# Optimization experiments

Measured on AMD Instinct MI355X. Metric: run time of the kernel, lower is better.

Reference implementation:

```python
import jax, jax.numpy as jnp
import numpy as np

N_NODES = 100_000
N_EDGES = 1_600_000
IN_CH = 16
OUT_CH = 64


def _init_linear(key, fan_in, fan_out):
    kw, kb = jax.random.split(key)
    bound = 1.0 / np.sqrt(fan_in)
    w = jax.random.uniform(kw, (fan_in, fan_out), jnp.float32, -bound, bound)
    b = jax.random.uniform(kb, (fan_out,), jnp.float32, -bound, bound)
    return w, b


def setup_inputs() -> dict:
    key = jax.random.key(0)
    ks = jax.random.split(key, 8)
    x = jax.random.normal(ks[0], (N_NODES, IN_CH), jnp.float32)
    pos = jax.random.normal(ks[1], (N_NODES, 3), jnp.float32)
    edge_index = jax.random.randint(ks[2], (2, N_EDGES), 0, N_NODES, jnp.int64)
    # local_nn: [in+3, 64, 128, out], ReLU after each linear
    w1, b1 = _init_linear(ks[3], IN_CH + 3, 64)
    w2, b2 = _init_linear(ks[4], 64, 128)
    w3, b3 = _init_linear(ks[5], 128, OUT_CH)
    # global_nn: [out, out]
    wg, bg = _init_linear(ks[6], OUT_CH, OUT_CH)
    return {"x": x, "pos": pos, "w1": w1, "b1": b1, "w2": w2, "b2": b2,
            "w3": w3, "b3": b3, "wg": wg, "bg": bg, "edge_index": edge_index}


def reference(x, pos, w1, b1, w2, b2, w3, b3, wg, bg, edge_index):
    src = edge_index[0]  # j (source / neighbor)
    dst = edge_index[1]  # i (target / center)
    # per-edge message input: [x_j, pos_j - pos_i]  -> [E, in+3]
    rel_pos = pos[src] - pos[dst]
    msg = jnp.concatenate([x[src], rel_pos], axis=-1)
    # local MLP (Linear -> ReLU chain)
    h = jax.nn.relu(msg @ w1 + b1)
    h = jax.nn.relu(h @ w2 + b2)
    h = jax.nn.relu(h @ w3 + b3)  # [E, out]
    # max aggregation over incoming edges per target node
    agg = jax.ops.segment_max(h, dst, num_segments=N_NODES)
    agg = jnp.where(jnp.isfinite(agg), agg, 0.0)  # isolated nodes -> 0
    # global MLP
    out = jax.nn.relu(agg @ wg + bg)  # [N, out]
    return out
```

## Files before the change

### kernel.cpp

```cpp
#include <hip/hip_runtime.h>


typedef __attribute__((ext_vector_type(8))) _Float16 half8;
typedef __attribute__((ext_vector_type(4))) float floatx4;

#define RELU(v) fmaxf((v), 0.0f)
#define LDS_FENCE() asm volatile("s_waitcnt lgkmcnt(0)" ::: "memory")

__global__ void count_prep_kernel(const int* __restrict__ ei, int E,
                                  int* __restrict__ cnt, int* __restrict__ rnk,
                                  const float* __restrict__ w1, const float* __restrict__ w2,
                                  const float* __restrict__ w3,
                                  _Float16* __restrict__ w1img, _Float16* __restrict__ w2img,
                                  _Float16* __restrict__ w3img)
{
    const int b = blockIdx.x;
    if (b < 8) {
        const int t = b * 256 + threadIdx.x;
        const int stride = 8 * 256;
        for (int i = t; i < 128 * 64; i += stride) {
            int o = i >> 6, cpr = (i >> 3) & 7, j = i & 7;
            int k = ((cpr ^ (o & 7)) << 3) | j;
            w2img[i] = (_Float16)w2[k * 128 + o];
        }
        for (int i = t; i < 64 * 128; i += stride) {
            int o = i >> 7, cpr = (i >> 3) & 15, j = i & 7;
            int kc = cpr ^ (o & 7);
            int k = (kc << 3) | j;
            w3img[i] = (_Float16)w3[k * 64 + o];
        }
        for (int i = t; i < 64 * 32; i += stride) {
            int o = i >> 5, c = (i >> 3) & 3, j = i & 7;
            int k = ((c ^ (o & 3)) << 3) | j;
            w1img[i] = (k < 19) ? (_Float16)w1[k * 64 + o] : (_Float16)0.0f;
        }
    } else {
        const int e = (b - 8) * 256 + threadIdx.x;
        if (e < E) rnk[e] = atomicAdd(&cnt[ei[E + e]], 1);
    }
}

__global__ __launch_bounds__(1024)
void scan1_kernel(const int* __restrict__ cnt, int* __restrict__ cur,
                  int* __restrict__ bsum, int N)
{
    __shared__ int sh[1024];
    const int t = threadIdx.x, b = blockIdx.x;
    const int idx = b * 1024 + t;
    int v = (idx < N) ? cnt[idx] : 0;
    sh[t] = v;
    __syncthreads();
    for (int off = 1; off < 1024; off <<= 1) {
        int o = (t >= off) ? sh[t - off] : 0;
        __syncthreads();
        sh[t] += o;
        __syncthreads();
    }
    if (idx < N) cur[idx] = sh[t] - v;
    if (t == 1023) bsum[b] = sh[t];
}

__global__ __launch_bounds__(128)
void scan2_kernel(int* __restrict__ bsum, int NB)
{
    __shared__ int sh[128];
    const int t = threadIdx.x;
    int v = (t < NB) ? bsum[t] : 0;
    sh[t] = v;
    __syncthreads();
    for (int off = 1; off < 128; off <<= 1) {
        int o = (t >= off) ? sh[t - off] : 0;
        __syncthreads();
        sh[t] += o;
        __syncthreads();
    }
    if (t < NB) bsum[t] = sh[t] - v;
}

__global__ void scatter_kernel(const int* __restrict__ ei, int E,
                               const int* __restrict__ cur, const int* __restrict__ bsum,
                               const int* __restrict__ rnk, int2* __restrict__ ep)
{
    int e = blockIdx.x * blockDim.x + threadIdx.x;
    if (e >= E) return;
    int s = ei[e], d = ei[E + e];
    int p = cur[d] + bsum[d >> 10] + rnk[e];
    ep[p] = make_int2(s, d);
}

__device__ __forceinline__ void load_msg(float* msg, int s, int d,
                                         const float* __restrict__ x,
                                         const float* __restrict__ pos)
{
    const float4* xv = reinterpret_cast<const float4*>(x + (size_t)s * 16);
    float4 x0 = xv[0], x1 = xv[1], x2 = xv[2], x3 = xv[3];
    msg[0] = x0.x;  msg[1] = x0.y;  msg[2] = x0.z;  msg[3] = x0.w;
    msg[4] = x1.x;  msg[5] = x1.y;  msg[6] = x1.z;  msg[7] = x1.w;
    msg[8] = x2.x;  msg[9] = x2.y;  msg[10] = x2.z; msg[11] = x2.w;
    msg[12] = x3.x; msg[13] = x3.y; msg[14] = x3.z; msg[15] = x3.w;
    msg[16] = pos[(size_t)s * 3 + 0] - pos[(size_t)d * 3 + 0];
    msg[17] = pos[(size_t)s * 3 + 1] - pos[(size_t)d * 3 + 1];
    msg[18] = pos[(size_t)s * 3 + 2] - pos[(size_t)d * 3 + 2];
}

__global__ __launch_bounds__(256, 2)
void edge_mlp_mfma(const float* __restrict__ x, const float* __restrict__ pos,
                   const _Float16* __restrict__ w1img, const float* __restrict__ b1,
                   const _Float16* __restrict__ w2img, const float* __restrict__ b2,
                   const _Float16* __restrict__ w3img, const float* __restrict__ b3,
                   const int2* __restrict__ ep, int E, float* __restrict__ aggf)
{
    __shared__ __align__(16) _Float16 w2s[128 * 64];
    __shared__ __align__(16) _Float16 w3s[64 * 128];
    __shared__ __align__(16) _Float16 w1s[64 * 32];
    __shared__ __align__(16) float b1s[64], b2s[128], b3s[64];
    __shared__ __align__(16) int2 sd[256];
    __shared__ __align__(16) float scratch[4][2048];

    const int t  = threadIdx.x;
    const int bs = blockIdx.x * 256;

    {
        const int4* s2 = (const int4*)w2img;
        int4* d2 = (int4*)w2s;
        for (int i = t; i < 1024; i += 256) d2[i] = s2[i];
        const int4* s3 = (const int4*)w3img;
        int4* d3 = (int4*)w3s;
        for (int i = t; i < 1024; i += 256) d3[i] = s3[i];
        const int4* s1 = (const int4*)w1img;
        int4* d1 = (int4*)w1s;
        if (t < 256) d1[t] = s1[t];
    }
    if (t < 64) { b1s[t] = b1[t]; b3s[t] = b3[t]; }
    if (t < 128) b2s[t] = b2[t];
    sd[t] = ep[min(bs + t, E - 1)];
    __syncthreads();

    const int lane = t & 63;
    const int w    = t >> 6;
    const int g    = lane >> 4;
    const int li   = lane & 15;
    const int W    = bs + w * 64;
    float*    h3w  = &scratch[w][0];
    _Float16* msgh = (_Float16*)&scratch[w][0];
    _Float16* h2h  = (_Float16*)&scratch[w][0];
    _Float16* h1s  = (_Float16*)&scratch[w][1024];

    const int n = min(64, E - W);
    const int c = lane;
    int prevd = -2, nextd = -2;
    if (n > 0) {
        prevd = (W == 0) ? -2 : __builtin_amdgcn_readfirstlane((w > 0) ? sd[w * 64 - 1].y : ep[W - 1].y);
        nextd = (W + n >= E) ? -2 : __builtin_amdgcn_readfirstlane((w < 3) ? sd[(w + 1) * 64].y : ep[W + 64].y);
    }
    int curd = -1;
    float mv = 0.0f;

    #pragma unroll
    for (int p = 0; p < 2; ++p) {
        if (lane < 32) {
            const int el = lane;
            int2 e0 = sd[w * 64 + p * 32 + el];
            float m[19];
            load_msg(m, e0.x, e0.y, x, pos);
            _Float16 hv[32];
            #pragma unroll
            for (int k = 0; k < 19; ++k) hv[k] = (_Float16)m[k];
            #pragma unroll
            for (int k = 19; k < 32; ++k) hv[k] = (_Float16)0.0f;
            const int sw = (el >> 1) & 3;
            #pragma unroll
            for (int cch = 0; cch < 4; ++cch) {
                half8 hh;
                #pragma unroll
                for (int j = 0; j < 8; ++j) hh[j] = hv[cch * 8 + j];
                *(half8*)&msgh[el * 32 + (cch ^ sw) * 8] = hh;
            }
        }
        LDS_FENCE();
        __builtin_amdgcn_sched_barrier(0);

        {
            half8 w1f[4];
            #pragma unroll
            for (int nf = 0; nf < 4; ++nf) {
                const int o = nf * 16 + li;
                w1f[nf] = *(const half8*)&w1s[o * 32 + (g ^ (o & 3)) * 8];
            }
            floatx4 acc1[2][4];
            #pragma unroll
            for (int nf = 0; nf < 4; ++nf) {
                float bv = b1s[nf * 16 + li];
                acc1[0][nf] = (floatx4){bv, bv, bv, bv};
                acc1[1][nf] = (floatx4){bv, bv, bv, bv};
            }
            #pragma unroll
            for (int mf = 0; mf < 2; ++mf) {
                const int el = mf * 16 + li;
                half8 af = *(const half8*)&msgh[el * 32 + (g ^ ((el >> 1) & 3)) * 8];
                #pragma unroll
                for (int nf = 0; nf < 4; ++nf)
                    acc1[mf][nf] = __builtin_amdgcn_mfma_f32_16x16x32_f16(af, w1f[nf], acc1[mf][nf], 0, 0, 0);
            }
            LDS_FENCE();
            #pragma unroll
            for (int mf = 0; mf < 2; ++mf)
                #pragma unroll
                for (int nf = 0; nf < 4; ++nf)
                    #pragma unroll
                    for (int r = 0; r < 4; ++r) {
                        const int e2 = mf * 16 + g * 4 + r;
                        const int o  = nf * 16 + li;
                        const int cpr = (o >> 3) ^ (e2 & 7);
                        h1s[e2 * 64 + cpr * 8 + (o & 7)] = (_Float16)RELU(acc1[mf][nf][r]);
                    }
        }
        LDS_FENCE();
        __builtin_amdgcn_sched_barrier(0);

        half8 afr[2][2];
        #pragma unroll
        for (int ks = 0; ks < 2; ++ks)
            #pragma unroll
            for (int mf = 0; mf < 2; ++mf) {
                const int e2 = mf * 16 + li;
                const int cpr = (ks * 4 + g) ^ (e2 & 7);
                afr[mf][ks] = *(const half8*)&h1s[e2 * 64 + cpr * 8];
            }

        floatx4 acc3[2][4];
        #pragma unroll
        for (int nf = 0; nf < 4; ++nf) {
            float bv = b3s[nf * 16 + li];
            acc3[0][nf] = (floatx4){bv, bv, bv, bv};
            acc3[1][nf] = (floatx4){bv, bv, bv, bv};
        }

        #pragma unroll
        for (int hf = 0; hf < 2; ++hf) {
            floatx4 acc2[2][4];
            #pragma unroll
            for (int nf = 0; nf < 4; ++nf) {
                float bv = b2s[hf * 64 + nf * 16 + li];
                acc2[0][nf] = (floatx4){bv, bv, bv, bv};
                acc2[1][nf] = (floatx4){bv, bv, bv, bv};
            }
            #pragma unroll
            for (int ks = 0; ks < 2; ++ks) {
                #pragma unroll
                for (int nf = 0; nf < 4; ++nf) {
                    const int o = hf * 64 + nf * 16 + li;
                    const int cpr = (ks * 4 + g) ^ (o & 7);
                    half8 bfr = *(const half8*)&w2s[o * 64 + cpr * 8];
                    acc2[0][nf] = __builtin_amdgcn_mfma_f32_16x16x32_f16(afr[0][ks], bfr, acc2[0][nf], 0, 0, 0);
                    acc2[1][nf] = __builtin_amdgcn_mfma_f32_16x16x32_f16(afr[1][ks], bfr, acc2[1][nf], 0, 0, 0);
                }
            }
            LDS_FENCE();
            #pragma unroll
            for (int mf = 0; mf < 2; ++mf)
                #pragma unroll
                for (int nf = 0; nf < 4; ++nf)
                    #pragma unroll
                    for (int r = 0; r < 4; ++r) {
                        const int e2 = mf * 16 + g * 4 + r;
                        const int ol = nf * 16 + li;
                        const int cpr = (ol >> 3) ^ (e2 & 7);
                        h2h[e2 * 64 + cpr * 8 + (ol & 7)] = (_Float16)RELU(acc2[mf][nf][r]);
                    }
            LDS_FENCE();
            __builtin_amdgcn_sched_barrier(0);
            #pragma unroll
            for (int ks_l = 0; ks_l < 2; ++ks_l) {
                const int ksg = hf * 2 + ks_l;
                half8 a2[2], b3f[4];
                #pragma unroll
                for (int mf = 0; mf < 2; ++mf) {
                    const int e2 = mf * 16 + li;
                    const int ca = (ks_l * 4 + g) ^ (e2 & 7);
                    a2[mf] = *(const half8*)&h2h[e2 * 64 + ca * 8];
                }
                #pragma unroll
                for (int nf = 0; nf < 4; ++nf) {
                    const int o = nf * 16 + li;
                    const int cb = (ksg * 4 + g) ^ (o & 7);
                    b3f[nf] = *(const half8*)&w3s[o * 128 + cb * 8];
                }
                #pragma unroll
                for (int mf = 0; mf < 2; ++mf)
                    #pragma unroll
                    for (int nf = 0; nf < 4; ++nf)
                        acc3[mf][nf] = __builtin_amdgcn_mfma_f32_16x16x32_f16(a2[mf], b3f[nf], acc3[mf][nf], 0, 0, 0);
            }
        }

        LDS_FENCE();
        #pragma unroll
        for (int mf = 0; mf < 2; ++mf)
            #pragma unroll
            for (int nf = 0; nf < 4; ++nf)
                #pragma unroll
                for (int r = 0; r < 4; ++r) {
                    const int e3 = mf * 16 + g * 4 + r;
                    const int o  = nf * 16 + li;
                    h3w[e3 * 64 + (o ^ (((e3 >> 2) & 3) << 4))] = RELU(acc3[mf][nf][r]);
                }
        LDS_FENCE();
        __builtin_amdgcn_sched_barrier(0);

        {
            const int lim = min(32, n - p * 32);
            for (int i = 0; i < lim; ++i) {
                const int d = __builtin_amdgcn_readfirstlane(sd[w * 64 + p * 32 + i].y);
                const float v = h3w[i * 64 + (c ^ (((i >> 2) & 3) << 4))];
                if (d != curd) {
                    if (curd >= 0) {
                        if (curd == prevd || curd == nextd)
                            atomicMax((int*)&aggf[(size_t)curd * 64 + c], __float_as_int(mv));
                        else
                            aggf[(size_t)curd * 64 + c] = mv;
                    }
                    curd = d;
                    mv = v;
                } else {
                    mv = fmaxf(mv, v);
                }
            }
        }
        LDS_FENCE();
    }

    if (curd >= 0) {
        if (curd == prevd || curd == nextd)
            atomicMax((int*)&aggf[(size_t)curd * 64 + c], __float_as_int(mv));
        else
            aggf[(size_t)curd * 64 + c] = mv;
    }
}

__global__ __launch_bounds__(256, 4)
void node_out_kernel(const float* __restrict__ agg, const float* __restrict__ wg,
                     const float* __restrict__ bg, float* __restrict__ out, int N)
{
    __shared__ float wgs[64 * 64];
    for (int i = threadIdx.x; i < 64 * 64; i += blockDim.x) wgs[i] = wg[i];
    __syncthreads();

    const int t = blockIdx.x * blockDim.x + threadIdx.x;
    const int nidx = t >> 4;
    const int og = t & 15;
    if (nidx >= N) return;

    const float4* aggv = reinterpret_cast<const float4*>(agg + (size_t)nidx * 64);
    const float4* wgsv = reinterpret_cast<const float4*>(wgs);

    float4 acc = reinterpret_cast<const float4*>(bg)[og];
    #pragma unroll
    for (int kg = 0; kg < 16; ++kg) {
        float4 a = aggv[kg];
        float4 w0 = wgsv[(kg * 4 + 0) * 16 + og];
        float4 w1 = wgsv[(kg * 4 + 1) * 16 + og];
        float4 w2 = wgsv[(kg * 4 + 2) * 16 + og];
        float4 w3 = wgsv[(kg * 4 + 3) * 16 + og];
        acc.x += a.x * w0.x + a.y * w1.x + a.z * w2.x + a.w * w3.x;
        acc.y += a.x * w0.y + a.y * w1.y + a.z * w2.y + a.w * w3.y;
        acc.z += a.x * w0.z + a.y * w1.z + a.z * w2.z + a.w * w3.z;
        acc.w += a.x * w0.w + a.y * w1.w + a.z * w2.w + a.w * w3.w;
    }
    float4 r;
    r.x = RELU(acc.x); r.y = RELU(acc.y); r.z = RELU(acc.z); r.w = RELU(acc.w);
    reinterpret_cast<float4*>(out)[(size_t)nidx * 16 + og] = r;
}

extern "C" void kernel_launch(void* const* d_in, const int* in_sizes, int n_in,
                              void* d_out, int out_size, void* d_ws, size_t ws_size,
                              hipStream_t stream)
{
    const float* x   = (const float*)d_in[0];
    const float* pos = (const float*)d_in[1];
    const float* w1  = (const float*)d_in[2];
    const float* b1  = (const float*)d_in[3];
    const float* w2  = (const float*)d_in[4];
    const float* b2  = (const float*)d_in[5];
    const float* w3  = (const float*)d_in[6];
    const float* b3  = (const float*)d_in[7];
    const float* wg  = (const float*)d_in[8];
    const float* bg  = (const float*)d_in[9];
    const int*   ei  = (const int*)d_in[10];

    const int N = in_sizes[0] / 16;
    const int E = in_sizes[10] / 2;

    int* wsi  = (int*)d_ws;
    int* cnt  = wsi;
    int* agg  = wsi + N;
    int* cur  = wsi + N + N * 64;
    int* bsum = wsi + N * 66;
    int2* ep  = (int2*)(wsi + N * 66 + 128);
    int* rnk  = wsi + N * 66 + 128 + 2 * E;
    _Float16* w2img = (_Float16*)(wsi + N * 66 + 128 + 3 * E);
    _Float16* w3img = w2img + 8192;
    _Float16* w1img = w3img + 8192;

    hipMemsetAsync(cnt, 0, (size_t)N * 65 * sizeof(int), stream);

    const int eb = (E + 255) / 256;
    const int NB = (N + 1023) / 1024;
    count_prep_kernel<<<eb + 8, 256, 0, stream>>>(ei, E, cnt, rnk,
                                                  w1, w2, w3, w1img, w2img, w3img);
    scan1_kernel<<<NB, 1024, 0, stream>>>(cnt, cur, bsum, N);
    scan2_kernel<<<1, 128, 0, stream>>>(bsum, NB);
    scatter_kernel<<<eb, 256, 0, stream>>>(ei, E, cur, bsum, rnk, ep);
    edge_mlp_mfma<<<(E + 255) / 256, 256, 0, stream>>>(
        x, pos, w1img, b1, w2img, b2, w3img, b3, ep, E, (float*)agg);
    node_out_kernel<<<(N * 16 + 255) / 256, 256, 0, stream>>>(
        (const float*)agg, wg, bg, (float*)d_out, N);
}
```

Measured before the change: 341.5 us.

## Use 1024-thread blocks, fp16 h3 scratch, and hoist weight/bias fragments to registers

Edge MLP blocks grow from 256 to 1024 threads (16 waves), so the LDS copy of the weights is amortized over four times as many edges. Per-wave scratch shrinks because layer-3 outputs are stored as packed fp16 pairs instead of fp32. W1 fragments and biases are loaded into registers once rather than on every pass. The risks are higher register pressure under the tighter launch bounds and a loss of precision in the max-aggregation values, which now pass through fp16.

```diff
diff --git a/kernel.cpp b/kernel.cpp
--- a/kernel.cpp
+++ b/kernel.cpp
@@ -2,6 +2,7 @@
 
 
 typedef __attribute__((ext_vector_type(8))) _Float16 half8;
+typedef __attribute__((ext_vector_type(2))) _Float16 half2v;
 typedef __attribute__((ext_vector_type(4))) float floatx4;
 
 #define RELU(v) fmaxf((v), 0.0f)
@@ -103,7 +104,7 @@
     msg[18] = pos[(size_t)s * 3 + 2] - pos[(size_t)d * 3 + 2];
 }
 
-__global__ __launch_bounds__(256, 2)
+__global__ __launch_bounds__(1024, 4)
 void edge_mlp_mfma(const float* __restrict__ x, const float* __restrict__ pos,
                    const _Float16* __restrict__ w1img, const float* __restrict__ b1,
                    const _Float16* __restrict__ w2img, const float* __restrict__ b2,
@@ -114,19 +115,19 @@
     __shared__ __align__(16) _Float16 w3s[64 * 128];
     __shared__ __align__(16) _Float16 w1s[64 * 32];
     __shared__ __align__(16) float b1s[64], b2s[128], b3s[64];
-    __shared__ __align__(16) int2 sd[256];
-    __shared__ __align__(16) float scratch[4][2048];
+    __shared__ __align__(16) int2 sd[1024];
+    __shared__ __align__(16) float scratch[16][1536];
 
     const int t  = threadIdx.x;
-    const int bs = blockIdx.x * 256;
+    const int bs = blockIdx.x * 1024;
 
     {
         const int4* s2 = (const int4*)w2img;
         int4* d2 = (int4*)w2s;
-        for (int i = t; i < 1024; i += 256) d2[i] = s2[i];
+        if (t < 1024) d2[t] = s2[t];
         const int4* s3 = (const int4*)w3img;
         int4* d3 = (int4*)w3s;
-        for (int i = t; i < 1024; i += 256) d3[i] = s3[i];
+        if (t < 1024) d3[t] = s3[t];
         const int4* s1 = (const int4*)w1img;
         int4* d1 = (int4*)w1s;
         if (t < 256) d1[t] = s1[t];
@@ -141,20 +142,32 @@
     const int g    = lane >> 4;
     const int li   = lane & 15;
     const int W    = bs + w * 64;
-    float*    h3w  = &scratch[w][0];
     _Float16* msgh = (_Float16*)&scratch[w][0];
+    _Float16* h1s  = (_Float16*)&scratch[w][512];
     _Float16* h2h  = (_Float16*)&scratch[w][0];
-    _Float16* h1s  = (_Float16*)&scratch[w][1024];
+    _Float16* h3h  = (_Float16*)&scratch[w][0];
 
     const int n = min(64, E - W);
     const int c = lane;
     int prevd = -2, nextd = -2;
     if (n > 0) {
         prevd = (W == 0) ? -2 : __builtin_amdgcn_readfirstlane((w > 0) ? sd[w * 64 - 1].y : ep[W - 1].y);
-        nextd = (W + n >= E) ? -2 : __builtin_amdgcn_readfirstlane((w < 3) ? sd[(w + 1) * 64].y : ep[W + 64].y);
+        nextd = (W + n >= E) ? -2 : __builtin_amdgcn_readfirstlane((w < 15) ? sd[(w + 1) * 64].y : ep[W + 64].y);
     }
     int curd = -1;
     float mv = 0.0f;
+
+    half8 w1f[4];
+    #pragma unroll
+    for (int nf = 0; nf < 4; ++nf) {
+        const int o = nf * 16 + li;
+        w1f[nf] = *(const half8*)&w1s[o * 32 + (g ^ (o & 3)) * 8];
+    }
+    float b1v[4], b2v[8], b3v[4];
+    #pragma unroll
+    for (int nf = 0; nf < 4; ++nf) { b1v[nf] = b1s[nf * 16 + li]; b3v[nf] = b3s[nf * 16 + li]; }
+    #pragma unroll
+    for (int i = 0; i < 8; ++i) b2v[i] = b2s[i * 16 + li];
 
     #pragma unroll
     for (int p = 0; p < 2; ++p) {
@@ -181,16 +194,10 @@
         __builtin_amdgcn_sched_barrier(0);
 
         {
-            half8 w1f[4];
+            floatx4 acc1[2][4];
             #pragma unroll
             for (int nf = 0; nf < 4; ++nf) {
-                const int o = nf * 16 + li;
-                w1f[nf] = *(const half8*)&w1s[o * 32 + (g ^ (o & 3)) * 8];
-            }
-            floatx4 acc1[2][4];
-            #pragma unroll
-            for (int nf = 0; nf < 4; ++nf) {
-                float bv = b1s[nf * 16 + li];
+                float bv = b1v[nf];
                 acc1[0][nf] = (floatx4){bv, bv, bv, bv};
                 acc1[1][nf] = (floatx4){bv, bv, bv, bv};
             }
@@ -231,7 +238,7 @@
         floatx4 acc3[2][4];
         #pragma unroll
         for (int nf = 0; nf < 4; ++nf) {
-            float bv = b3s[nf * 16 + li];
+            float bv = b3v[nf];
             acc3[0][nf] = (floatx4){bv, bv, bv, bv};
             acc3[1][nf] = (floatx4){bv, bv, bv, bv};
         }
@@ -241,7 +248,7 @@
             floatx4 acc2[2][4];
             #pragma unroll
             for (int nf = 0; nf < 4; ++nf) {
-                float bv = b2s[hf * 64 + nf * 16 + li];
+                float bv = b2v[hf * 4 + nf];
                 acc2[0][nf] = (floatx4){bv, bv, bv, bv};
                 acc2[1][nf] = (floatx4){bv, bv, bv, bv};
             }
@@ -298,13 +305,17 @@
         #pragma unroll
         for (int mf = 0; mf < 2; ++mf)
             #pragma unroll
-            for (int nf = 0; nf < 4; ++nf)
-                #pragma unroll
-                for (int r = 0; r < 4; ++r) {
-                    const int e3 = mf * 16 + g * 4 + r;
-                    const int o  = nf * 16 + li;
-                    h3w[e3 * 64 + (o ^ (((e3 >> 2) & 3) << 4))] = RELU(acc3[mf][nf][r]);
+            for (int nf = 0; nf < 4; ++nf) {
+                const int o = nf * 16 + li;
+                #pragma unroll
+                for (int q = 0; q < 2; ++q) {
+                    const int pr = mf * 8 + g * 2 + q;
+                    half2v pk;
+                    pk.x = (_Float16)RELU(acc3[mf][nf][q * 2]);
+                    pk.y = (_Float16)RELU(acc3[mf][nf][q * 2 + 1]);
+                    *(half2v*)&h3h[(pr * 64 + o) * 2] = pk;
                 }
+            }
         LDS_FENCE();
         __builtin_amdgcn_sched_barrier(0);
 
@@ -312,7 +323,7 @@
             const int lim = min(32, n - p * 32);
             for (int i = 0; i < lim; ++i) {
                 const int d = __builtin_amdgcn_readfirstlane(sd[w * 64 + p * 32 + i].y);
-                const float v = h3w[i * 64 + (c ^ (((i >> 2) & 3) << 4))];
+                const float v = (float)h3h[((i >> 1) * 64 + c) * 2 + (i & 1)];
                 if (d != curd) {
                     if (curd >= 0) {
                         if (curd == prevd || curd == nextd)
@@ -411,7 +422,7 @@
     scan1_kernel<<<NB, 1024, 0, stream>>>(cnt, cur, bsum, N);
     scan2_kernel<<<1, 128, 0, stream>>>(bsum, NB);
     scatter_kernel<<<eb, 256, 0, stream>>>(ei, E, cur, bsum, rnk, ep);
-    edge_mlp_mfma<<<(E + 255) / 256, 256, 0, stream>>>(
+    edge_mlp_mfma<<<(E + 1023) / 1024, 1024, 0, stream>>>(
         x, pos, w1img, b1, w2img, b2, w3img, b3, ep, E, (float*)agg);
     node_out_kernel<<<(N * 16 + 255) / 256, 256, 0, stream>>>(
         (const float*)agg, wg, bg, (float*)d_out, N);
```

Result: slower. 525.2 us (+53.8%).
